# Performance work log

Hardware: AMD Instinct MI355X
Metric: run time of the kernel (lower is better)

The kernel has to match this reference:

```python
import jax, jax.numpy as jnp
import numpy as np

B, S, H = 4, 2048, 1024
NH, HD = 16, 64
ROPE_THETA = 160000.0
SCALE = HD ** -0.5


def _rope_cos_sin(position_ids, dim, theta):
    # neox-style rotary: frequencies over half the head dim
    inv_freq = 1.0 / (theta ** (jnp.arange(0, dim, 2, dtype=jnp.float32) / dim))  # [dim/2]
    freqs = position_ids.astype(jnp.float32)[..., None] * inv_freq  # [B,S,dim/2]
    return jnp.cos(freqs), jnp.sin(freqs)


def _apply_rope(x, cos, sin):
    # x: [B,S,NH,HD]; neox style: rotate halves
    d2 = x.shape[-1] // 2
    x1, x2 = x[..., :d2], x[..., d2:]
    c = cos[:, :, None, :]
    s = sin[:, :, None, :]
    return jnp.concatenate([x1 * c - x2 * s, x2 * c + x1 * s], axis=-1)


def setup_inputs() -> dict:
    key = jax.random.key(0)
    k1, k2, k3 = jax.random.split(key, 3)
    hidden_states = jax.random.normal(k1, (B, S, H), dtype=jnp.float32)
    position_ids = jnp.tile(jnp.arange(S, dtype=jnp.int32)[None, :], (B, 1))
    Wqkv = jax.random.normal(k2, (3 * H, H), dtype=jnp.float32) * (H ** -0.5)
    Wo = jax.random.normal(k3, (H, H), dtype=jnp.float32) * (H ** -0.5)
    return {"hidden_states": hidden_states, "position_ids": position_ids,
            "Wqkv": Wqkv, "Wo": Wo}


def reference(hidden_states, position_ids, Wqkv, Wo):
    # fused QKV projection
    qkv = jnp.einsum('bsh,oh->bso', hidden_states, Wqkv)  # [B,S,3H]
    q, k, v = jnp.split(qkv, 3, axis=-1)
    q = q.reshape(B, S, NH, HD)
    k = k.reshape(B, S, NH, HD)
    v = v.reshape(B, S, NH, HD)
    # rotary embedding (neox style)
    cos, sin = _rope_cos_sin(position_ids, HD, ROPE_THETA)
    q = _apply_rope(q, cos, sin)
    k = _apply_rope(k, cos, sin)
    # full bidirectional (encoder-only, global layer) attention
    scores = jnp.einsum('bqhd,bkhd->bhqk', q, k) * SCALE  # [B,NH,S,S]
    probs = jax.nn.softmax(scores, axis=-1)
    ctx = jnp.einsum('bhqk,bkhd->bqhd', probs, v).reshape(B, S, H)
    # output projection
    return jnp.einsum('bsh,oh->bso', ctx, Wo)
```

## Files before the change

### kernel.cpp

```cpp
#include <hip/hip_runtime.h>
#include <hip/hip_bf16.h>


#define GLOBAL_AS __attribute__((address_space(1)))
#define LDS_AS    __attribute__((address_space(3)))

using f32x4  = __attribute__((ext_vector_type(4))) float;
using f32x16 = __attribute__((ext_vector_type(16))) float;
using s16x8  = __attribute__((ext_vector_type(8))) short;

__device__ __forceinline__ void gld_lds16(const void* g, void* l) {
  __builtin_amdgcn_global_load_lds((const GLOBAL_AS void*)g, (LDS_AS void*)l, 16, 0, 0);
}

__device__ __forceinline__ unsigned short f2bf(float f) {
  unsigned int u = __float_as_uint(f);
  u = (u + 0x7fffu + ((u >> 16) & 1u)) >> 16;
  return (unsigned short)u;
}
__device__ __forceinline__ unsigned int cvt_pk_bf16(float lo, float hi) {
  unsigned int r;
  asm("v_cvt_pk_bf16_f32 %0, %1, %2" : "=v"(r) : "v"(lo), "v"(hi));
  return r;
}
__device__ __forceinline__ void pswap(unsigned int& a, unsigned int& b) {
  asm("v_permlane32_swap_b32 %0, %1" : "+v"(a), "+v"(b));
}

__global__ __launch_bounds__(256) void cvt_rope_kernel(const float* __restrict__ h,
                                                       const float* __restrict__ wq,
                                                       const float* __restrict__ wo,
                                                       const int* __restrict__ pos,
                                                       unsigned short* __restrict__ hb,
                                                       unsigned short* __restrict__ wqb,
                                                       unsigned short* __restrict__ wob,
                                                       float* __restrict__ ctab,
                                                       float* __restrict__ stab) {
  int b = blockIdx.x;
  if (b >= 12288) {
    int idx = (b - 12288) * 256 + threadIdx.x;
    int d = idx & 31;
    int bs = idx >> 5;
    float p = (float)pos[bs];
    float inv = exp2f(-(float)d * 0.5402410118609203f);
    float f = p * inv;
    ctab[idx] = cosf(f);
    stab[idx] = sinf(f);
    return;
  }
  const float* src; unsigned short* dst; int i;
  if (b < 8192)       { src = h;  dst = hb;  i = b * 256 + threadIdx.x; }
  else if (b < 11264) { src = wq; dst = wqb; i = (b - 8192) * 256 + threadIdx.x; }
  else                { src = wo; dst = wob; i = (b - 11264) * 256 + threadIdx.x; }
  float4 v = ((const float4*)src)[i];
  ushort4 o;
  o.x = f2bf(v.x); o.y = f2bf(v.y); o.z = f2bf(v.z); o.w = f2bf(v.w);
  ((ushort4*)dst)[i] = o;
}

template<int MODE>
__global__ __launch_bounds__(256) void gemm_bt_kernel(const unsigned short* __restrict__ A,
                                                      const unsigned short* __restrict__ Bm,
                                                      void* __restrict__ C, int N, int K,
                                                      const float* __restrict__ ctab,
                                                      const float* __restrict__ stab,
                                                      unsigned short* __restrict__ Qr,
                                                      unsigned short* __restrict__ Kr,
                                                      unsigned short* __restrict__ Vt) {
  __shared__ char sAB[32768];
  char* sA = sAB;
  char* sB = sAB + 16384;
  const int tid  = threadIdx.x;
  const int lane = tid & 63, w = tid >> 6;
  const int g = lane >> 4, c = lane & 15;
  const int wr = w >> 1, wc = w & 1;
  const int m0 = blockIdx.x * 128, n0 = blockIdx.y * 128;
  const char* Ab = (const char*)A;
  const char* Bb = (const char*)Bm;

  f32x4 acc[4][4] = {};
  for (int k0 = 0; k0 < K; k0 += 64) {
    __syncthreads();
#pragma unroll
    for (int rr = 0; rr < 4; ++rr) {
      int o = tid * 16 + rr * 4096;
      int row = o >> 7;
      int col = (o & 127) ^ ((row & 7) << 4);
      gld_lds16(Ab + ((size_t)(m0 + row) * K + k0) * 2 + col, sA + o);
      gld_lds16(Bb + ((size_t)(n0 + row) * K + k0) * 2 + col, sB + o);
    }
    __syncthreads();
#pragma unroll
    for (int ks = 0; ks < 2; ++ks) {
      s16x8 af[4], bfr[4];
#pragma unroll
      for (int i = 0; i < 4; ++i) {
        int row = 64 * wr + 16 * i + c;
        af[i] = *(const s16x8*)(sA + ((row * 128 + ks * 64 + g * 16) ^ ((row & 7) << 4)));
      }
#pragma unroll
      for (int j = 0; j < 4; ++j) {
        int row = 64 * wc + 16 * j + c;
        bfr[j] = *(const s16x8*)(sB + ((row * 128 + ks * 64 + g * 16) ^ ((row & 7) << 4)));
      }
#pragma unroll
      for (int i = 0; i < 4; ++i)
#pragma unroll
        for (int j = 0; j < 4; ++j)
          acc[i][j] = __builtin_amdgcn_mfma_f32_16x16x32_bf16(af[i], bfr[j], acc[i][j], 0, 0, 0);
    }
  }

  if (MODE == 1) {
#pragma unroll
    for (int i = 0; i < 4; ++i)
#pragma unroll
      for (int j = 0; j < 4; ++j)
#pragma unroll
        for (int r = 0; r < 4; ++r) {
          int m = m0 + 64 * wr + 16 * i + 4 * g + r;
          int n = n0 + 64 * wc + 16 * j + c;
          ((float*)C)[(size_t)m * N + n] = acc[i][j][r];
        }
  } else {
    const int t = blockIdx.y;
    if (t < 16) {
      unsigned short* dstb = (t < 8) ? Qr : Kr;
      const float qs = (t < 8) ? 0.18033688011112042f : 1.0f;
      const int h = 2 * (t & 7) + wc;
#pragma unroll
      for (int i = 0; i < 4; ++i)
#pragma unroll
        for (int r = 0; r < 4; ++r) {
          int m = m0 + 64 * wr + 16 * i + 4 * g + r;
          int b = m >> 11, s = m & 2047;
          unsigned short* drow = dstb + ((size_t)(b * 16 + h) * 2048 + s) * 64;
#pragma unroll
          for (int j = 0; j < 2; ++j) {
            int d = 16 * j + c;
            float co = ctab[(size_t)m * 32 + d];
            float si = stab[(size_t)m * 32 + d];
            float x1 = acc[i][j][r], x2 = acc[i][j + 2][r];
            drow[d]      = f2bf((x1 * co - x2 * si) * qs);
            drow[d + 32] = f2bf((x2 * co + x1 * si) * qs);
          }
        }
    } else {
      unsigned short (*tile)[74] = (unsigned short (*)[74])sAB;
      const int bb = m0 >> 11, sb = m0 & 2047;
#pragma unroll
      for (int hp = 0; hp < 2; ++hp) {
        __syncthreads();
        if (wc == hp) {
#pragma unroll
          for (int i = 0; i < 4; ++i)
#pragma unroll
            for (int j = 0; j < 4; ++j)
#pragma unroll
              for (int r = 0; r < 4; ++r)
                tile[64 * wr + 16 * i + 4 * g + r][16 * j + c] = f2bf(acc[i][j][r]);
        }
        __syncthreads();
        int h = (t - 16) * 2 + hp;
        int p = tid & 7;
#pragma unroll
        for (int dd = 0; dd < 2; ++dd) {
          int d = (tid >> 3) + 32 * dd;
          alignas(16) unsigned short vv[16];
#pragma unroll
          for (int i2 = 0; i2 < 16; ++i2) vv[i2] = tile[p * 16 + i2][d];
          unsigned short* dst = Vt + ((size_t)(bb * 16 + h) * 64 + d) * 2048 + sb + p * 16;
          *(uint4*)dst       = ((const uint4*)vv)[0];
          *(uint4*)(dst + 8) = ((const uint4*)vv)[1];
        }
      }
    }
  }
}

__global__ __launch_bounds__(512) void attn_kernel(const unsigned short* __restrict__ Q,
                                                   const unsigned short* __restrict__ Kr,
                                                   const unsigned short* __restrict__ Vt,
                                                   unsigned short* __restrict__ Ctx) {
  __shared__ char sK[3][8192];
  __shared__ char sV[3][8192];
  const int tid  = threadIdx.x;
  const int lane = tid & 63, w = tid >> 6;
  const int hi = lane >> 5, ql = lane & 31;
  const int swz = (ql & 7) << 4;
  int lin = blockIdx.x + 8 * blockIdx.y;
  int eff = (lin & 7) * 64 + (lin >> 3);
  const int bh = eff >> 3;
  const int q0 = (eff & 7) * 256;
  const char* kh = (const char*)(Kr + (size_t)bh * 2048 * 64);
  const char* vh = (const char*)(Vt + (size_t)bh * 64 * 2048);

  s16x8 qf[4];
  {
    const char* qrow = (const char*)Q + ((size_t)bh * 2048 + q0 + 32 * w + ql) * 128;
#pragma unroll
    for (int t = 0; t < 4; ++t) qf[t] = *(const s16x8*)(qrow + t * 32 + hi * 16);
  }
  __builtin_amdgcn_sched_barrier(0);

#define STAGE(t, b)                                                              \
  {                                                                              \
    int o = tid * 16;                                                            \
    int l = o ^ (((o >> 7) & 7) << 4);                                           \
    gld_lds16(kh + (size_t)(t) * 8192 + l, sK[b] + o);                           \
    gld_lds16(vh + (size_t)(o >> 7) * 4096 + (t) * 128 + (l & 127), sV[b] + o);  \
  }

  STAGE(0, 0);
  __builtin_amdgcn_sched_barrier(0);
  STAGE(1, 1);
  __builtin_amdgcn_sched_barrier(0);

  float l_run = 0.f;
  f32x16 oa0 = {}, oa1 = {};
  int cur = 0;

  for (int it = 0; it < 32; ++it) {
    if (it == 0 || it == 31) asm volatile("s_waitcnt vmcnt(0)" ::: "memory");
    else                     asm volatile("s_waitcnt vmcnt(2)" ::: "memory");
    __builtin_amdgcn_sched_barrier(0);
    __builtin_amdgcn_s_barrier();
    __builtin_amdgcn_sched_barrier(0);

    if (it + 2 < 32) {
      int sb = cur + 2; if (sb >= 3) sb -= 3;
      STAGE(it + 2, sb);
    }
    __builtin_amdgcn_sched_barrier(0);

    f32x16 sc0 = {}, sc1 = {};
    __builtin_amdgcn_s_setprio(1);
#pragma unroll
    for (int t = 0; t < 4; ++t) {
      int cx = (t * 32 + hi * 16) ^ swz;
      s16x8 k0 = *(const s16x8*)(sK[cur] + ql * 128 + cx);
      s16x8 k1 = *(const s16x8*)(sK[cur] + (32 + ql) * 128 + cx);
      sc0 = __builtin_amdgcn_mfma_f32_32x32x16_bf16(k0, qf[t], sc0, 0, 0, 0);
      sc1 = __builtin_amdgcn_mfma_f32_32x32x16_bf16(k1, qf[t], sc1, 0, 0, 0);
    }
    __builtin_amdgcn_s_setprio(0);

    float rs = 0.f;
#pragma unroll
    for (int r = 0; r < 16; ++r) { sc0[r] = __builtin_amdgcn_exp2f(sc0[r]); rs += sc0[r]; }
#pragma unroll
    for (int r = 0; r < 16; ++r) { sc1[r] = __builtin_amdgcn_exp2f(sc1[r]); rs += sc1[r]; }
    l_run += rs;

    unsigned int bp[16];
#pragma unroll
    for (int blk = 0; blk < 2; ++blk) {
      const f32x16& s = blk ? sc1 : sc0;
      unsigned int a0 = cvt_pk_bf16(s[0],  s[1]);
      unsigned int a1 = cvt_pk_bf16(s[2],  s[3]);
      unsigned int a2 = cvt_pk_bf16(s[4],  s[5]);
      unsigned int a3 = cvt_pk_bf16(s[6],  s[7]);
      pswap(a0, a2); pswap(a1, a3);
      bp[blk * 8 + 0] = a0; bp[blk * 8 + 1] = a1;
      bp[blk * 8 + 2] = a2; bp[blk * 8 + 3] = a3;
      unsigned int b0 = cvt_pk_bf16(s[8],  s[9]);
      unsigned int b1 = cvt_pk_bf16(s[10], s[11]);
      unsigned int b2 = cvt_pk_bf16(s[12], s[13]);
      unsigned int b3 = cvt_pk_bf16(s[14], s[15]);
      pswap(b0, b2); pswap(b1, b3);
      bp[blk * 8 + 4] = b0; bp[blk * 8 + 5] = b1;
      bp[blk * 8 + 6] = b2; bp[blk * 8 + 7] = b3;
    }

    __builtin_amdgcn_s_setprio(1);
#pragma unroll
    for (int ss = 0; ss < 4; ++ss) {
      uint4 u = {bp[ss * 4], bp[ss * 4 + 1], bp[ss * 4 + 2], bp[ss * 4 + 3]};
      s16x8 pb = __builtin_bit_cast(s16x8, u);
      int cx = (ss * 32 + hi * 16) ^ swz;
      s16x8 v0 = *(const s16x8*)(sV[cur] + ql * 128 + cx);
      s16x8 v1 = *(const s16x8*)(sV[cur] + (32 + ql) * 128 + cx);
      oa0 = __builtin_amdgcn_mfma_f32_32x32x16_bf16(v0, pb, oa0, 0, 0, 0);
      oa1 = __builtin_amdgcn_mfma_f32_32x32x16_bf16(v1, pb, oa1, 0, 0, 0);
    }
    __builtin_amdgcn_s_setprio(0);

    ++cur; if (cur == 3) cur = 0;
  }
#undef STAGE

  l_run += __shfl_xor(l_run, 32);
  float inv = 1.f / l_run;
  const int b = bh >> 4, h = bh & 15;
  const int q = q0 + 32 * w + ql;
  unsigned short* crow = Ctx + ((size_t)(b * 2048 + q)) * 1024 + h * 64;
#pragma unroll
  for (int dblk = 0; dblk < 2; ++dblk) {
    const f32x16& oa = dblk ? oa1 : oa0;
#pragma unroll
    for (int grp = 0; grp < 4; ++grp) {
      ushort4 st;
      st.x = f2bf(oa[4 * grp + 0] * inv);
      st.y = f2bf(oa[4 * grp + 1] * inv);
      st.z = f2bf(oa[4 * grp + 2] * inv);
      st.w = f2bf(oa[4 * grp + 3] * inv);
      *(ushort4*)(crow + dblk * 32 + 8 * grp + 4 * hi) = st;
    }
  }
}

extern "C" void kernel_launch(void* const* d_in, const int* in_sizes, int n_in,
                              void* d_out, int out_size, void* d_ws, size_t ws_size,
                              hipStream_t stream) {
  const float* hidden = (const float*)d_in[0];
  const int*   pos    = (const int*)d_in[1];
  const float* wqkv   = (const float*)d_in[2];
  const float* wo     = (const float*)d_in[3];

  char* ws = (char*)d_ws;
  unsigned short* hbf  = (unsigned short*)(ws);
  unsigned short* wqbf = (unsigned short*)(ws + 16777216);
  unsigned short* wobf = (unsigned short*)(ws + 23068672);
  unsigned short* Qr   = (unsigned short*)(ws + 41943040);
  unsigned short* Kr   = (unsigned short*)(ws + 58720256);
  unsigned short* Vt   = (unsigned short*)(ws + 75497472);
  unsigned short* ctx  = (unsigned short*)(ws + 92274688);
  float*          ctab = (float*)(ws + 109051904);
  float*          stab = (float*)(ws + 110100480);

  cvt_rope_kernel<<<13312, 256, 0, stream>>>(hidden, wqkv, wo, pos,
                                             hbf, wqbf, wobf, ctab, stab);

  dim3 gq(64, 24);
  gemm_bt_kernel<2><<<gq, 256, 0, stream>>>(hbf, wqbf, nullptr, 3072, 1024,
                                            ctab, stab, Qr, Kr, Vt);

  dim3 ga(8, 64);
  attn_kernel<<<ga, 512, 0, stream>>>(Qr, Kr, Vt, ctx);

  dim3 go(64, 8);
  gemm_bt_kernel<1><<<go, 256, 0, stream>>>(ctx, wobf, d_out, 1024, 1024,
                                            nullptr, nullptr, nullptr, nullptr, nullptr);
}
```

Baseline: 187.9 us.

## Double-buffer GEMM with 256x128 tiles, 512 threads, and async LDS prefetch

Replaces the single-buffered 128x128 GEMM with a 256x128-tile, 8-wave kernel that double-buffers A/B in 96KB of dynamic LDS. It prefetches the next k-tile with global_load_lds and uses vmcnt waits, raw s_barrier and setprio around the MFMA block. The goal is to hide global-load latency behind MFMA work and raise B-tile reuse. The V-transpose epilogue now writes 32 positions per thread. The cost is high LDS use, which limits occupancy, and fewer blocks on the small output GEMM.

```diff
diff --git a/kernel.cpp b/kernel.cpp
--- a/kernel.cpp
+++ b/kernel.cpp
@@ -59,57 +59,104 @@
 }
 
 template<int MODE>
-__global__ __launch_bounds__(256) void gemm_bt_kernel(const unsigned short* __restrict__ A,
-                                                      const unsigned short* __restrict__ Bm,
-                                                      void* __restrict__ C, int N, int K,
-                                                      const float* __restrict__ ctab,
-                                                      const float* __restrict__ stab,
-                                                      unsigned short* __restrict__ Qr,
-                                                      unsigned short* __restrict__ Kr,
-                                                      unsigned short* __restrict__ Vt) {
-  __shared__ char sAB[32768];
-  char* sA = sAB;
-  char* sB = sAB + 16384;
+__global__ __launch_bounds__(512) void gemm2_kernel(const unsigned short* __restrict__ A,
+                                                    const unsigned short* __restrict__ Bm,
+                                                    void* __restrict__ C, int N, int K,
+                                                    const float* __restrict__ ctab,
+                                                    const float* __restrict__ stab,
+                                                    unsigned short* __restrict__ Qr,
+                                                    unsigned short* __restrict__ Kr,
+                                                    unsigned short* __restrict__ Vt) {
+  extern __shared__ char lds[];
   const int tid  = threadIdx.x;
   const int lane = tid & 63, w = tid >> 6;
   const int g = lane >> 4, c = lane & 15;
   const int wr = w >> 1, wc = w & 1;
-  const int m0 = blockIdx.x * 128, n0 = blockIdx.y * 128;
+  const int m0 = blockIdx.x * 256, n0 = blockIdx.y * 128;
   const char* Ab = (const char*)A;
   const char* Bb = (const char*)Bm;
+  const int NKT = K >> 6;
+
+#define STAGE_A(kt, hh)                                                          \
+  {                                                                              \
+    _Pragma("unroll")                                                            \
+    for (int L = 0; L < 2; ++L) {                                                \
+      int o = tid * 16 + L * 8192;                                               \
+      int row = o >> 7;                                                          \
+      int gcol = (o & 127) ^ ((row & 7) << 4);                                   \
+      gld_lds16(Ab + ((size_t)(m0 + (hh) * 128 + row) * K + (kt) * 64) * 2 + gcol,\
+                lds + ((kt) & 1) * 49152 + (hh) * 16384 + o);                    \
+    }                                                                            \
+  }
+#define STAGE_B(kt, hh)                                                          \
+  {                                                                              \
+    int o = tid * 16;                                                            \
+    int row = o >> 7;                                                            \
+    int gcol = (o & 127) ^ ((row & 7) << 4);                                     \
+    gld_lds16(Bb + ((size_t)(n0 + (hh) * 64 + row) * K + (kt) * 64) * 2 + gcol,  \
+              lds + ((kt) & 1) * 49152 + 32768 + (hh) * 8192 + o);               \
+  }
+
+  STAGE_A(0, 0); STAGE_B(0, 0); STAGE_A(0, 1); STAGE_B(0, 1);
+  __builtin_amdgcn_sched_barrier(0);
+  STAGE_A(1, 0); STAGE_B(1, 0);
+  __builtin_amdgcn_sched_barrier(0);
 
   f32x4 acc[4][4] = {};
-  for (int k0 = 0; k0 < K; k0 += 64) {
-    __syncthreads();
-#pragma unroll
-    for (int rr = 0; rr < 4; ++rr) {
-      int o = tid * 16 + rr * 4096;
-      int row = o >> 7;
-      int col = (o & 127) ^ ((row & 7) << 4);
-      gld_lds16(Ab + ((size_t)(m0 + row) * K + k0) * 2 + col, sA + o);
-      gld_lds16(Bb + ((size_t)(n0 + row) * K + k0) * 2 + col, sB + o);
-    }
-    __syncthreads();
-#pragma unroll
-    for (int ks = 0; ks < 2; ++ks) {
-      s16x8 af[4], bfr[4];
-#pragma unroll
-      for (int i = 0; i < 4; ++i) {
-        int row = 64 * wr + 16 * i + c;
-        af[i] = *(const s16x8*)(sA + ((row * 128 + ks * 64 + g * 16) ^ ((row & 7) << 4)));
-      }
-#pragma unroll
-      for (int j = 0; j < 4; ++j) {
-        int row = 64 * wc + 16 * j + c;
-        bfr[j] = *(const s16x8*)(sB + ((row * 128 + ks * 64 + g * 16) ^ ((row & 7) << 4)));
-      }
+  const int rA0 = (wr & 1) * 64 + c;
+  for (int kt = 0; kt < NKT; ++kt) {
+    if (kt == NKT - 1) asm volatile("s_waitcnt vmcnt(0)" ::: "memory");
+    else               asm volatile("s_waitcnt vmcnt(3)" ::: "memory");
+    __builtin_amdgcn_sched_barrier(0);
+    __builtin_amdgcn_s_barrier();
+    __builtin_amdgcn_sched_barrier(0);
+
+    const char* baseA = lds + (kt & 1) * 49152 + (wr >> 1) * 16384;
+    const char* baseB = lds + (kt & 1) * 49152 + 32768 + wc * 8192;
+
+    s16x8 af[4][2], bf[4][2];
+#pragma unroll
+    for (int i = 0; i < 4; ++i) {
+      int row = rA0 + 16 * i;
+#pragma unroll
+      for (int ks = 0; ks < 2; ++ks)
+        af[i][ks] = *(const s16x8*)(baseA + ((row * 128 + ks * 64 + g * 16) ^ ((row & 7) << 4)));
+    }
+#pragma unroll
+    for (int j = 0; j < 4; ++j) {
+      int row = 16 * j + c;
+#pragma unroll
+      for (int ks = 0; ks < 2; ++ks)
+        bf[j][ks] = *(const s16x8*)(baseB + ((row * 128 + ks * 64 + g * 16) ^ ((row & 7) << 4)));
+    }
+
+    if (kt + 1 < NKT) {
+      STAGE_A(kt + 1, 1);
+      STAGE_B(kt + 1, 1);
+    }
+    __builtin_amdgcn_sched_barrier(0);
+
+    __builtin_amdgcn_s_setprio(1);
+#pragma unroll
+    for (int ks = 0; ks < 2; ++ks)
 #pragma unroll
       for (int i = 0; i < 4; ++i)
 #pragma unroll
         for (int j = 0; j < 4; ++j)
-          acc[i][j] = __builtin_amdgcn_mfma_f32_16x16x32_bf16(af[i], bfr[j], acc[i][j], 0, 0, 0);
-    }
-  }
+          acc[i][j] = __builtin_amdgcn_mfma_f32_16x16x32_bf16(af[i][ks], bf[j][ks], acc[i][j], 0, 0, 0);
+    __builtin_amdgcn_s_setprio(0);
+
+    __builtin_amdgcn_sched_barrier(0);
+    __builtin_amdgcn_s_barrier();
+    __builtin_amdgcn_sched_barrier(0);
+    if (kt + 2 < NKT) {
+      STAGE_A(kt + 2, 0);
+      STAGE_B(kt + 2, 0);
+      __builtin_amdgcn_sched_barrier(0);
+    }
+  }
+#undef STAGE_A
+#undef STAGE_B
 
   if (MODE == 1) {
 #pragma unroll
@@ -118,8 +165,8 @@
       for (int j = 0; j < 4; ++j)
 #pragma unroll
         for (int r = 0; r < 4; ++r) {
-          int m = m0 + 64 * wr + 16 * i + 4 * g + r;
-          int n = n0 + 64 * wc + 16 * j + c;
+          int m = m0 + wr * 64 + 16 * i + 4 * g + r;
+          int n = n0 + wc * 64 + 16 * j + c;
           ((float*)C)[(size_t)m * N + n] = acc[i][j][r];
         }
   } else {
@@ -132,7 +179,7 @@
       for (int i = 0; i < 4; ++i)
 #pragma unroll
         for (int r = 0; r < 4; ++r) {
-          int m = m0 + 64 * wr + 16 * i + 4 * g + r;
+          int m = m0 + wr * 64 + 16 * i + 4 * g + r;
           int b = m >> 11, s = m & 2047;
           unsigned short* drow = dstb + ((size_t)(b * 16 + h) * 2048 + s) * 64;
 #pragma unroll
@@ -146,7 +193,7 @@
           }
         }
     } else {
-      unsigned short (*tile)[74] = (unsigned short (*)[74])sAB;
+      unsigned short (*tile)[72] = (unsigned short (*)[72])lds;
       const int bb = m0 >> 11, sb = m0 & 2047;
 #pragma unroll
       for (int hp = 0; hp < 2; ++hp) {
@@ -158,21 +205,18 @@
             for (int j = 0; j < 4; ++j)
 #pragma unroll
               for (int r = 0; r < 4; ++r)
-                tile[64 * wr + 16 * i + 4 * g + r][16 * j + c] = f2bf(acc[i][j][r]);
+                tile[wr * 64 + 16 * i + 4 * g + r][16 * j + c] = f2bf(acc[i][j][r]);
         }
         __syncthreads();
-        int h = (t - 16) * 2 + hp;
-        int p = tid & 7;
-#pragma unroll
-        for (int dd = 0; dd < 2; ++dd) {
-          int d = (tid >> 3) + 32 * dd;
-          alignas(16) unsigned short vv[16];
-#pragma unroll
-          for (int i2 = 0; i2 < 16; ++i2) vv[i2] = tile[p * 16 + i2][d];
-          unsigned short* dst = Vt + ((size_t)(bb * 16 + h) * 64 + d) * 2048 + sb + p * 16;
-          *(uint4*)dst       = ((const uint4*)vv)[0];
-          *(uint4*)(dst + 8) = ((const uint4*)vv)[1];
-        }
+        int hh = 2 * (t - 16) + hp;
+        int d = tid >> 3, p = tid & 7;
+        alignas(16) unsigned short vv[32];
+#pragma unroll
+        for (int i2 = 0; i2 < 32; ++i2) vv[i2] = tile[p * 32 + i2][d];
+        unsigned short* dst = Vt + ((size_t)(bb * 16 + hh) * 64 + d) * 2048 + sb + p * 32;
+#pragma unroll
+        for (int q4 = 0; q4 < 4; ++q4)
+          *(uint4*)(dst + 8 * q4) = ((const uint4*)vv)[q4];
       }
     }
   }
@@ -331,14 +375,14 @@
   cvt_rope_kernel<<<13312, 256, 0, stream>>>(hidden, wqkv, wo, pos,
                                              hbf, wqbf, wobf, ctab, stab);
 
-  dim3 gq(64, 24);
-  gemm_bt_kernel<2><<<gq, 256, 0, stream>>>(hbf, wqbf, nullptr, 3072, 1024,
-                                            ctab, stab, Qr, Kr, Vt);
+  dim3 gq(32, 24);
+  gemm2_kernel<2><<<gq, 512, 98304, stream>>>(hbf, wqbf, nullptr, 3072, 1024,
+                                              ctab, stab, Qr, Kr, Vt);
 
   dim3 ga(8, 64);
   attn_kernel<<<ga, 512, 0, stream>>>(Qr, Kr, Vt, ctx);
 
-  dim3 go(64, 8);
-  gemm_bt_kernel<1><<<go, 256, 0, stream>>>(ctx, wobf, d_out, 1024, 1024,
-                                            nullptr, nullptr, nullptr, nullptr, nullptr);
-}
+  dim3 go(32, 8);
+  gemm2_kernel<1><<<go, 512, 98304, stream>>>(ctx, wobf, d_out, 1024, 1024,
+                                              nullptr, nullptr, nullptr, nullptr, nullptr);
+}
```

After: 184.9 us. Within noise of the previous version (-1.6%).
